# Kernel optimization log

Measured on AMD Instinct MI355X. Metric: run time of the kernel, lower is better.

## Reference

```python
import jax, jax.numpy as jnp
import numpy as np

N = 4096
D = 2048
NUM_CLASSES = 128
MARGIN = 0.5


def setup_inputs() -> dict:
    key = jax.random.key(0)
    k1, k2, k3 = jax.random.split(key, 3)
    modal1_inputs = jax.random.normal(k1, (N, D), dtype=jnp.float32)
    modal2_inputs = jax.random.normal(k2, (N, D), dtype=jnp.float32)
    targets = jax.random.randint(k3, (N,), 0, NUM_CLASSES, dtype=jnp.int32)
    return {"modal1_inputs": modal1_inputs, "modal2_inputs": modal2_inputs, "targets": targets}


def _segment_mean(x, seg_ids, num_segments):
    sums = jax.ops.segment_sum(x, seg_ids, num_segments=num_segments)
    cnts = jax.ops.segment_sum(jnp.ones((x.shape[0],), x.dtype), seg_ids, num_segments=num_segments)
    return sums / jnp.maximum(cnts, 1.0)[:, None]


def _pairwise_dist(a, b):
    # sqrt of clamped squared Euclidean distance, matching compute_dist
    sq = (jnp.sum(a * a, axis=1)[:, None] + jnp.sum(b * b, axis=1)[None, :]
          - 2.0 * jnp.einsum('nd,md->nm', a, b))
    return jnp.sqrt(jnp.maximum(sq, 1e-12))


def _contrastive(d2, d1, label, margin):
    # mean(label * d2^2 + (1-label) * relu(margin - d1)^2)
    return jnp.mean(label * d2 * d2
                    + (1.0 - label) * jnp.square(jnp.maximum(margin - d1, 0.0)))


def reference(modal1_inputs, modal2_inputs, targets):
    # per-label means (segment mean), gathered back per-sample as in the loop
    meanR = _segment_mean(modal1_inputs, targets, NUM_CLASSES)  # [C, D]
    meanT = _segment_mean(modal2_inputs, targets, NUM_CLASSES)  # [C, D]
    centersR = meanR[targets]                                   # [N, D]
    centersT = meanT[targets]                                   # [N, D]
    centers = 0.5 * (centersR + centersT)                       # [N, D]

    label = (targets[:, None] == targets[None, :]).astype(jnp.float32)  # [N, N]

    dist1 = _pairwise_dist(centersR, centers)  # already sqrt'ed, per original
    dist2 = _pairwise_dist(centersT, centers)
    dd1 = jnp.sqrt(dist1 + 1e-10)              # sqrt of sqrt, per original
    dd2 = jnp.sqrt(dist2 + 1e-10)

    loss1 = _contrastive(dist1, dd1, label, MARGIN)
    loss2 = _contrastive(dist2, dd2, label, MARGIN)
    return loss1 + loss2
```

## Files before the change

### kernel.cpp

```cpp
#include <hip/hip_runtime.h>

#define N_SAMPLES 4096
#define DIM 2048
#define NUM_CLASSES 128
#define MARGIN 0.5f


__global__ __launch_bounds__(256) void mean_kernel(
        const float* __restrict__ x1,
        const float* __restrict__ x2,
        const int* __restrict__ targets,
        int* __restrict__ cnt,
        float* __restrict__ meanR,
        float* __restrict__ meanT,
        float* __restrict__ d_out, int out_size) {
    __shared__ int s_rows[N_SAMPLES];
    __shared__ int s_n;
    const int tid = threadIdx.x;
    const int c = blockIdx.y;
    const float* __restrict__ x = (blockIdx.z == 0) ? x1 : x2;
    float* __restrict__ mean    = (blockIdx.z == 0) ? meanR : meanT;

    if (tid == 0) s_n = 0;
    if (blockIdx.x == 0 && blockIdx.y == 0 && blockIdx.z == 0) {
        for (int i = tid; i < out_size; i += 256) d_out[i] = 0.0f;
    }
    __syncthreads();

    const int4* __restrict__ t4 = (const int4*)targets;
    for (int i = tid; i < N_SAMPLES / 4; i += 256) {
        const int4 v = t4[i];
        const int base = i * 4;
        if (v.x == c) s_rows[atomicAdd(&s_n, 1)] = base;
        if (v.y == c) s_rows[atomicAdd(&s_n, 1)] = base + 1;
        if (v.z == c) s_rows[atomicAdd(&s_n, 1)] = base + 2;
        if (v.w == c) s_rows[atomicAdd(&s_n, 1)] = base + 3;
    }
    __syncthreads();
    const int n = s_n;

    const int col = blockIdx.x * 256 + tid;
    const float4* __restrict__ xs = (const float4*)x;
    float ax = 0.0f, ay = 0.0f, az = 0.0f, aw = 0.0f;

#define LOADG(B, g) do {                                               \
        const int _base = (g) * 8;                                     \
        _Pragma("unroll")                                              \
        for (int u = 0; u < 8; ++u) {                                  \
            const int _r = s_rows[_base + u];                          \
            B[u] = xs[(size_t)_r * (DIM / 4) + col];                   \
        }                                                              \
    } while (0)

#define ACCG(B) do {                                                   \
        _Pragma("unroll")                                              \
        for (int u = 0; u < 8; ++u) {                                  \
            ax += B[u].x; ay += B[u].y; az += B[u].z; aw += B[u].w;    \
        }                                                              \
    } while (0)

    const int nfull = n >> 3;
    const int rem   = n & 7;

    float4 T[8];
    if (rem) {
        const int tbase = nfull * 8;
#pragma unroll
        for (int u = 0; u < 8; ++u) {
            const int idx = tbase + ((u < rem) ? u : 0);
            T[u] = xs[(size_t)s_rows[idx] * (DIM / 4) + col];
        }
    }

    if (nfull > 0) {
        float4 bufA[8], bufB[8];
        LOADG(bufA, 0);
        int g = 1;
        for (; g + 1 < nfull; g += 2) {
            LOADG(bufB, g);
            ACCG(bufA);
            LOADG(bufA, g + 1);
            ACCG(bufB);
        }
        if (g < nfull) {
            LOADG(bufB, g);
            ACCG(bufA);
            ACCG(bufB);
        } else {
            ACCG(bufA);
        }
    }

    if (rem) {
#pragma unroll
        for (int u = 0; u < 8; ++u) {
            const float m = (u < rem) ? 1.0f : 0.0f;
            ax = fmaf(T[u].x, m, ax);
            ay = fmaf(T[u].y, m, ay);
            az = fmaf(T[u].z, m, az);
            aw = fmaf(T[u].w, m, aw);
        }
    }
#undef LOADG
#undef ACCG

    const float inv = 1.0f / (float)((n > 0) ? n : 1);
    float4 m; m.x = ax * inv; m.y = ay * inv; m.z = az * inv; m.w = aw * inv;
    ((float4*)mean)[(size_t)c * (DIM / 4) + col] = m;

    if (blockIdx.x == 0 && blockIdx.z == 0 && tid == 0) cnt[c] = n;
}

__device__ __forceinline__ void accum_sq(float& acc, const float4& a, const float4& c) {
    float d;
    d = a.x - c.x; acc = fmaf(d, d, acc);
    d = a.y - c.y; acc = fmaf(d, d, acc);
    d = a.z - c.z; acc = fmaf(d, d, acc);
    d = a.w - c.w; acc = fmaf(d, d, acc);
}

__device__ __forceinline__ float wave_sum64(float v) {
#pragma unroll
    for (int m = 32; m >= 1; m >>= 1) v += __shfl_xor(v, m, 64);
    return v;
}

__global__ __launch_bounds__(256) void loss_kernel(
        const float* __restrict__ meanR,
        const float* __restrict__ meanT,
        const int* __restrict__ cnt,
        float* __restrict__ d_out) {
    const int tile = blockIdx.x;
    const int a0 = (tile >> 5) * 4;
    const int b0 = (tile & 31) * 4;
    const int wave = threadIdx.x >> 6;
    const int lane = threadIdx.x & 63;

    float acc1[4][4], acc2[4][4];
#pragma unroll
    for (int i = 0; i < 4; ++i)
#pragma unroll
        for (int j = 0; j < 4; ++j) { acc1[i][j] = 0.0f; acc2[i][j] = 0.0f; }

#pragma unroll
    for (int it = 0; it < 2; ++it) {
        const int d = wave * 128 + it * 64 + lane;
        float4 ra[4], ta[4];
#pragma unroll
        for (int i = 0; i < 4; ++i) {
            ra[i] = ((const float4*)(meanR + (size_t)(a0 + i) * DIM))[d];
            ta[i] = ((const float4*)(meanT + (size_t)(a0 + i) * DIM))[d];
        }
#pragma unroll
        for (int j = 0; j < 4; ++j) {
            const int b = b0 + j;
            const float4 rb = ((const float4*)(meanR + (size_t)b * DIM))[d];
            const float4 tb = ((const float4*)(meanT + (size_t)b * DIM))[d];
            float4 cb;
            cb.x = 0.5f * (rb.x + tb.x);
            cb.y = 0.5f * (rb.y + tb.y);
            cb.z = 0.5f * (rb.z + tb.z);
            cb.w = 0.5f * (rb.w + tb.w);
#pragma unroll
            for (int i = 0; i < 4; ++i) {
                accum_sq(acc1[i][j], ra[i], cb);
                accum_sq(acc2[i][j], ta[i], cb);
            }
        }
    }

#pragma unroll
    for (int i = 0; i < 4; ++i)
#pragma unroll
        for (int j = 0; j < 4; ++j) {
            acc1[i][j] = wave_sum64(acc1[i][j]);
            acc2[i][j] = wave_sum64(acc2[i][j]);
        }

    __shared__ float s1[4][16], s2[4][16];
    if (lane == 0) {
#pragma unroll
        for (int i = 0; i < 4; ++i)
#pragma unroll
            for (int j = 0; j < 4; ++j) {
                s1[wave][i * 4 + j] = acc1[i][j];
                s2[wave][i * 4 + j] = acc2[i][j];
            }
    }
    __syncthreads();

    if (threadIdx.x < 64) {
        float total = 0.0f;
        if (threadIdx.x < 16) {
            const int idx = threadIdx.x;
            const int i = idx >> 2, j = idx & 3;
            const int a = a0 + i, b = b0 + j;
            const float sqa1 = (s1[0][idx] + s1[1][idx]) + (s1[2][idx] + s1[3][idx]);
            const float sqa2 = (s2[0][idx] + s2[1][idx]) + (s2[2][idx] + s2[3][idx]);
            const float invN2 = 1.0f / ((float)N_SAMPLES * (float)N_SAMPLES);
            const float w = (float)cnt[a] * (float)cnt[b] * invN2;
            const float sq1 = fmaxf(sqa1, 1e-12f);
            const float sq2 = fmaxf(sqa2, 1e-12f);
            float t1, t2;
            if (a == b) {
                t1 = sq1;
                t2 = sq2;
            } else {
                const float dd1 = sqrtf(sqrtf(sq1) + 1e-10f);
                const float dd2 = sqrtf(sqrtf(sq2) + 1e-10f);
                const float r1 = fmaxf(MARGIN - dd1, 0.0f);
                const float r2 = fmaxf(MARGIN - dd2, 0.0f);
                t1 = r1 * r1;
                t2 = r2 * r2;
            }
            total = w * (t1 + t2);
        }
        total = wave_sum64(total);
        if (threadIdx.x == 0) atomicAdd(d_out, total);
    }
}

extern "C" void kernel_launch(void* const* d_in, const int* in_sizes, int n_in,
                              void* d_out, int out_size, void* d_ws, size_t ws_size,
                              hipStream_t stream) {
    const float* modal1 = (const float*)d_in[0];
    const float* modal2 = (const float*)d_in[1];
    const int* targets  = (const int*)d_in[2];
    float* out = (float*)d_out;

    char* ws = (char*)d_ws;
    int*   cnt   = (int*)(ws + 0);
    float* meanR = (float*)(ws + 1024);
    float* meanT = (float*)(ws + 1024 + (size_t)NUM_CLASSES * DIM * 4);

    dim3 gridB(2, NUM_CLASSES, 2);
    mean_kernel<<<gridB, 256, 0, stream>>>(modal1, modal2, targets, cnt,
                                           meanR, meanT, out, out_size);

    loss_kernel<<<NUM_CLASSES / 4 * NUM_CLASSES / 4, 256, 0, stream>>>(
        meanR, meanT, cnt, out);
}
```

Measured before the change: 115.6 us.

## Prune off-diagonal pair distances with a norm-based triangle-inequality bound

Adds a per-class stats kernel that computes the norms of the R, T and center means, plus the closed-form diagonal distance (a quarter of ||R-T||^2). The pair kernel then skips the full distance computation for any pair whose norm difference already proves the distance exceeds margin^4, since those pairs contribute zero hinge loss. Surviving pairs fall back to a scalar per-thread loop over the 2048-long dimension with uncoalesced loads. This trades the dense 128x128 distance tile for one extra launch and a data-dependent slow path. With random Gaussian inputs, the class means have norms near 4 and distances far above 0.0625, so nearly every off-diagonal pair is skipped.

```diff
diff --git a/kernel.cpp b/kernel.cpp
--- a/kernel.cpp
+++ b/kernel.cpp
@@ -111,113 +111,102 @@
     if (blockIdx.x == 0 && blockIdx.z == 0 && tid == 0) cnt[c] = n;
 }
 
-__device__ __forceinline__ void accum_sq(float& acc, const float4& a, const float4& c) {
-    float d;
-    d = a.x - c.x; acc = fmaf(d, d, acc);
-    d = a.y - c.y; acc = fmaf(d, d, acc);
-    d = a.z - c.z; acc = fmaf(d, d, acc);
-    d = a.w - c.w; acc = fmaf(d, d, acc);
-}
-
 __device__ __forceinline__ float wave_sum64(float v) {
 #pragma unroll
     for (int m = 32; m >= 1; m >>= 1) v += __shfl_xor(v, m, 64);
     return v;
 }
 
-__global__ __launch_bounds__(256) void loss_kernel(
+__global__ __launch_bounds__(256) void stat_kernel(
         const float* __restrict__ meanR,
         const float* __restrict__ meanT,
+        float* __restrict__ stats) {
+    const int c = blockIdx.x;
+    const int tid = threadIdx.x;
+    const float4* __restrict__ r4 = (const float4*)(meanR + (size_t)c * DIM);
+    const float4* __restrict__ t4 = (const float4*)(meanT + (size_t)c * DIM);
+    float sr = 0.0f, st = 0.0f, sc = 0.0f, sd = 0.0f;
+    for (int i = tid; i < DIM / 4; i += 256) {
+        const float4 r = r4[i], t = t4[i];
+        float cx, dx;
+#define DO(f) cx = 0.5f * (r.f + t.f); dx = r.f - t.f;               \
+        sr = fmaf(r.f, r.f, sr); st = fmaf(t.f, t.f, st);            \
+        sc = fmaf(cx, cx, sc);   sd = fmaf(dx, dx, sd);
+        DO(x) DO(y) DO(z) DO(w)
+#undef DO
+    }
+    sr = wave_sum64(sr); st = wave_sum64(st);
+    sc = wave_sum64(sc); sd = wave_sum64(sd);
+    __shared__ float s[4][4];
+    const int wave = tid >> 6;
+    if ((tid & 63) == 0) {
+        s[wave][0] = sr; s[wave][1] = st; s[wave][2] = sc; s[wave][3] = sd;
+    }
+    __syncthreads();
+    if (tid < 4) {
+        float v = (s[0][tid] + s[1][tid]) + (s[2][tid] + s[3][tid]);
+        v = (tid < 3) ? sqrtf(v) : 0.25f * v;
+        stats[tid * NUM_CLASSES + c] = v;
+    }
+}
+
+__global__ __launch_bounds__(256) void pair_kernel(
+        const float* __restrict__ meanR,
+        const float* __restrict__ meanT,
+        const float* __restrict__ stats,
         const int* __restrict__ cnt,
         float* __restrict__ d_out) {
-    const int tile = blockIdx.x;
-    const int a0 = (tile >> 5) * 4;
-    const int b0 = (tile & 31) * 4;
-    const int wave = threadIdx.x >> 6;
-    const int lane = threadIdx.x & 63;
-
-    float acc1[4][4], acc2[4][4];
-#pragma unroll
-    for (int i = 0; i < 4; ++i)
-#pragma unroll
-        for (int j = 0; j < 4; ++j) { acc1[i][j] = 0.0f; acc2[i][j] = 0.0f; }
-
-#pragma unroll
-    for (int it = 0; it < 2; ++it) {
-        const int d = wave * 128 + it * 64 + lane;
-        float4 ra[4], ta[4];
-#pragma unroll
-        for (int i = 0; i < 4; ++i) {
-            ra[i] = ((const float4*)(meanR + (size_t)(a0 + i) * DIM))[d];
-            ta[i] = ((const float4*)(meanT + (size_t)(a0 + i) * DIM))[d];
-        }
-#pragma unroll
-        for (int j = 0; j < 4; ++j) {
-            const int b = b0 + j;
-            const float4 rb = ((const float4*)(meanR + (size_t)b * DIM))[d];
-            const float4 tb = ((const float4*)(meanT + (size_t)b * DIM))[d];
-            float4 cb;
-            cb.x = 0.5f * (rb.x + tb.x);
-            cb.y = 0.5f * (rb.y + tb.y);
-            cb.z = 0.5f * (rb.z + tb.z);
-            cb.w = 0.5f * (rb.w + tb.w);
-#pragma unroll
-            for (int i = 0; i < 4; ++i) {
-                accum_sq(acc1[i][j], ra[i], cb);
-                accum_sq(acc2[i][j], ta[i], cb);
+    const int idx = blockIdx.x * 256 + threadIdx.x;
+    const int a = idx >> 7;
+    const int b = idx & 127;
+    const float* __restrict__ rn  = stats;
+    const float* __restrict__ tn  = stats + NUM_CLASSES;
+    const float* __restrict__ cn  = stats + 2 * NUM_CLASSES;
+    const float* __restrict__ sqd = stats + 3 * NUM_CLASSES;
+
+    const float invN2 = 1.0f / ((float)N_SAMPLES * (float)N_SAMPLES);
+    const float w = (float)cnt[a] * (float)cnt[b] * invN2;
+
+    float total;
+    if (a == b) {
+        const float t = fmaxf(sqd[a], 1e-12f);
+        total = w * (t + t);
+    } else {
+        const float THR = MARGIN * MARGIN * MARGIN * MARGIN;
+        const float g1 = rn[a] - cn[b];
+        const float g2 = tn[a] - cn[b];
+        float t1 = 0.0f, t2 = 0.0f;
+        if ((g1 * g1 < THR) | (g2 * g2 < THR)) {
+            float sq1 = 0.0f, sq2 = 0.0f;
+            const float* __restrict__ ra = meanR + (size_t)a * DIM;
+            const float* __restrict__ ta = meanT + (size_t)a * DIM;
+            const float* __restrict__ rb = meanR + (size_t)b * DIM;
+            const float* __restrict__ tb = meanT + (size_t)b * DIM;
+            for (int k = 0; k < DIM; ++k) {
+                const float cb = 0.5f * (rb[k] + tb[k]);
+                const float e1 = ra[k] - cb;
+                const float e2 = ta[k] - cb;
+                sq1 = fmaf(e1, e1, sq1);
+                sq2 = fmaf(e2, e2, sq2);
             }
-        }
-    }
-
-#pragma unroll
-    for (int i = 0; i < 4; ++i)
-#pragma unroll
-        for (int j = 0; j < 4; ++j) {
-            acc1[i][j] = wave_sum64(acc1[i][j]);
-            acc2[i][j] = wave_sum64(acc2[i][j]);
-        }
-
-    __shared__ float s1[4][16], s2[4][16];
-    if (lane == 0) {
-#pragma unroll
-        for (int i = 0; i < 4; ++i)
-#pragma unroll
-            for (int j = 0; j < 4; ++j) {
-                s1[wave][i * 4 + j] = acc1[i][j];
-                s2[wave][i * 4 + j] = acc2[i][j];
-            }
-    }
-    __syncthreads();
-
-    if (threadIdx.x < 64) {
-        float total = 0.0f;
-        if (threadIdx.x < 16) {
-            const int idx = threadIdx.x;
-            const int i = idx >> 2, j = idx & 3;
-            const int a = a0 + i, b = b0 + j;
-            const float sqa1 = (s1[0][idx] + s1[1][idx]) + (s1[2][idx] + s1[3][idx]);
-            const float sqa2 = (s2[0][idx] + s2[1][idx]) + (s2[2][idx] + s2[3][idx]);
-            const float invN2 = 1.0f / ((float)N_SAMPLES * (float)N_SAMPLES);
-            const float w = (float)cnt[a] * (float)cnt[b] * invN2;
-            const float sq1 = fmaxf(sqa1, 1e-12f);
-            const float sq2 = fmaxf(sqa2, 1e-12f);
-            float t1, t2;
-            if (a == b) {
-                t1 = sq1;
-                t2 = sq2;
-            } else {
-                const float dd1 = sqrtf(sqrtf(sq1) + 1e-10f);
-                const float dd2 = sqrtf(sqrtf(sq2) + 1e-10f);
-                const float r1 = fmaxf(MARGIN - dd1, 0.0f);
-                const float r2 = fmaxf(MARGIN - dd2, 0.0f);
-                t1 = r1 * r1;
-                t2 = r2 * r2;
-            }
-            total = w * (t1 + t2);
-        }
-        total = wave_sum64(total);
-        if (threadIdx.x == 0) atomicAdd(d_out, total);
-    }
+            sq1 = fmaxf(sq1, 1e-12f);
+            sq2 = fmaxf(sq2, 1e-12f);
+            const float dd1 = sqrtf(sqrtf(sq1) + 1e-10f);
+            const float dd2 = sqrtf(sqrtf(sq2) + 1e-10f);
+            const float r1 = fmaxf(MARGIN - dd1, 0.0f);
+            const float r2 = fmaxf(MARGIN - dd2, 0.0f);
+            t1 = r1 * r1;
+            t2 = r2 * r2;
+        }
+        total = w * (t1 + t2);
+    }
+
+    total = wave_sum64(total);
+    __shared__ float sp[4];
+    if ((threadIdx.x & 63) == 0) sp[threadIdx.x >> 6] = total;
+    __syncthreads();
+    if (threadIdx.x == 0)
+        atomicAdd(d_out, (sp[0] + sp[1]) + (sp[2] + sp[3]));
 }
 
 extern "C" void kernel_launch(void* const* d_in, const int* in_sizes, int n_in,
@@ -232,11 +221,14 @@
     int*   cnt   = (int*)(ws + 0);
     float* meanR = (float*)(ws + 1024);
     float* meanT = (float*)(ws + 1024 + (size_t)NUM_CLASSES * DIM * 4);
+    float* stats = (float*)(ws + 1024 + 2 * (size_t)NUM_CLASSES * DIM * 4);
 
     dim3 gridB(2, NUM_CLASSES, 2);
     mean_kernel<<<gridB, 256, 0, stream>>>(modal1, modal2, targets, cnt,
                                            meanR, meanT, out, out_size);
 
-    loss_kernel<<<NUM_CLASSES / 4 * NUM_CLASSES / 4, 256, 0, stream>>>(
-        meanR, meanT, cnt, out);
-}
+    stat_kernel<<<NUM_CLASSES, 256, 0, stream>>>(meanR, meanT, stats);
+
+    pair_kernel<<<(NUM_CLASSES * NUM_CLASSES) / 256, 256, 0, stream>>>(
+        meanR, meanT, stats, cnt, out);
+}
```

Result: slower. 204.4 us (+76.9%).
